# Optimization experiments

Hardware: AMD Instinct MI355X
Metric: run time of the kernel (lower is better)

Reference implementation:

```python
import jax, jax.numpy as jnp
import numpy as np

HEADS = 8
DIM_HEAD = 64
SCALE = DIM_HEAD ** -0.5

B, N, DIM = 4096, 16, 512  # (batch*spatial, frames, channels)
HIDDEN = HEADS * DIM_HEAD  # 512


def setup_inputs() -> dict:
    key = jax.random.key(0)
    k1, k2, k3 = jax.random.split(key, 3)
    x = jax.random.normal(k1, (B, N, DIM), dtype=jnp.float32)
    # torch Linear(dim, 3*hidden, bias=False) applied as x @ W^T; we store the
    # transposed weight directly so forward is x @ w_qkv.
    w_qkv = jax.random.normal(k2, (DIM, 3 * HIDDEN), dtype=jnp.float32) * (DIM ** -0.5)
    w_out = jax.random.normal(k3, (HIDDEN, DIM), dtype=jnp.float32) * (HIDDEN ** -0.5)
    return {"x": x, "w_qkv": w_qkv, "w_out": w_out}


def reference(x, w_qkv, w_out):
    # qkv projection and split
    qkv = x @ w_qkv                                   # [b, n, 3*hidden]
    q, k, v = jnp.split(qkv, 3, axis=-1)              # each [b, n, hidden]

    def to_heads(t):
        b, n, _ = t.shape
        return t.reshape(b, n, HEADS, DIM_HEAD).transpose(0, 2, 1, 3)  # [b, h, n, d]

    q, k, v = to_heads(q), to_heads(k), to_heads(v)

    # linear attention feature maps
    q = jax.nn.softmax(q, axis=-1) * SCALE            # softmax over d
    k = jax.nn.softmax(k, axis=-2)                    # softmax over n

    # context = k^T v : [b, h, d, e]
    context = jnp.einsum('bhnd,bhne->bhde', k, v)
    out = jnp.einsum('bhnd,bhde->bhne', q, context)   # [b, h, n, e]

    b = out.shape[0]
    out = out.transpose(0, 2, 1, 3).reshape(b, N, HIDDEN)  # [b, n, hidden]
    return out @ w_out
```

## Files before the change

### kernel.cpp

```cpp
#include <hip/hip_runtime.h>
#include <hip/hip_bf16.h>


typedef __attribute__((ext_vector_type(8))) short bf16x8;
typedef __attribute__((ext_vector_type(4))) float f32x4;

__device__ __forceinline__ unsigned short f2bf(float f) {
  __hip_bfloat16 h = __float2bfloat16(f);
  return __builtin_bit_cast(unsigned short, h);
}
__device__ __forceinline__ float bf2f(unsigned short u) {
  unsigned int v = ((unsigned int)u) << 16;
  return __builtin_bit_cast(float, v);
}
__device__ __forceinline__ void gload16(const void* g, void* l) {
  __builtin_amdgcn_global_load_lds(
      (__attribute__((address_space(1))) void*)g,
      (__attribute__((address_space(3))) void*)l, 16, 0, 0);
}

__global__ __launch_bounds__(256) void conv_x_k(const float* __restrict__ x,
                                                unsigned short* __restrict__ xb) {
  size_t i = ((size_t)blockIdx.x * 256 + threadIdx.x) * 8;
  float4 a = *(const float4*)(x + i);
  float4 b = *(const float4*)(x + i + 4);
  union { unsigned short u[8]; bf16x8 v; } o;
  o.u[0] = f2bf(a.x); o.u[1] = f2bf(a.y); o.u[2] = f2bf(a.z); o.u[3] = f2bf(a.w);
  o.u[4] = f2bf(b.x); o.u[5] = f2bf(b.y); o.u[6] = f2bf(b.z); o.u[7] = f2bf(b.w);
  *(bf16x8*)(xb + i) = o.v;
}

__global__ __launch_bounds__(256) void conv_w_k(const float* __restrict__ wq,
                                                const float* __restrict__ wo,
                                                unsigned short* __restrict__ wqt,
                                                unsigned short* __restrict__ wot) {
  int i = blockIdx.x * 256 + threadIdx.x;
  if (i < 786432) {
    int n = i >> 9, k = i & 511;
    wqt[i] = f2bf(wq[k * 1536 + n]);
  } else {
    int j = i - 786432;
    int n = j >> 9, k = j & 511;
    wot[j] = f2bf(wo[k * 512 + n]);
  }
}

__global__ __launch_bounds__(256) void gemm_qkv_k(const unsigned short* __restrict__ A,
                                                  const unsigned short* __restrict__ B,
                                                  unsigned short* __restrict__ C) {
  __shared__ __align__(16) unsigned short As[128 * 32];
  __shared__ __align__(16) unsigned short Bs[128 * 32];
  int orig = blockIdx.x;
  int local = orig >> 3;
  int mtile = (orig & 7) * 64 + local / 12;
  int ntile = local % 12;
  int m0 = mtile * 128, n0 = ntile * 128;
  int tid = threadIdx.x, w = tid >> 6, l = tid & 63;
  int wr = w >> 1, wc = w & 1;

  f32x4 z4 = {0.f, 0.f, 0.f, 0.f};
  f32x4 acc[4][4];
#pragma unroll
  for (int i = 0; i < 4; ++i)
#pragma unroll
    for (int j = 0; j < 4; ++j) acc[i][j] = z4;

  const unsigned short* ga0 = A + (size_t)(m0 + w * 32 + (l >> 2)) * 512 + (l & 3) * 8;
  const unsigned short* gb0 = B + (size_t)(n0 + w * 32 + (l >> 2)) * 512 + (l & 3) * 8;
  unsigned short* lA = &As[(w * 32) * 32];
  unsigned short* lB = &Bs[(w * 32) * 32];

  for (int kb = 0; kb < 16; ++kb) {
    if (kb) __syncthreads();
    const unsigned short* ga = ga0 + kb * 32;
    const unsigned short* gb = gb0 + kb * 32;
    gload16(ga, lA);
    gload16(ga + 16 * 512, lA + 16 * 32);
    gload16(gb, lB);
    gload16(gb + 16 * 512, lB + 16 * 32);
    __syncthreads();

    bf16x8 af[4], bfr[4];
#pragma unroll
    for (int mt = 0; mt < 4; ++mt)
      af[mt] = *(const bf16x8*)&As[(wr * 64 + mt * 16 + (l & 15)) * 32 + (l >> 4) * 8];
#pragma unroll
    for (int nt = 0; nt < 4; ++nt)
      bfr[nt] = *(const bf16x8*)&Bs[(wc * 64 + nt * 16 + (l & 15)) * 32 + (l >> 4) * 8];
#pragma unroll
    for (int mt = 0; mt < 4; ++mt)
#pragma unroll
      for (int nt = 0; nt < 4; ++nt)
        acc[mt][nt] = __builtin_amdgcn_mfma_f32_16x16x32_bf16(af[mt], bfr[nt], acc[mt][nt], 0, 0, 0);
  }

#pragma unroll
  for (int mt = 0; mt < 4; ++mt)
#pragma unroll
    for (int nt = 0; nt < 4; ++nt)
#pragma unroll
      for (int r = 0; r < 4; ++r) {
        int row = m0 + wr * 64 + mt * 16 + (l >> 4) * 4 + r;
        int col = n0 + wc * 64 + nt * 16 + (l & 15);
        C[(size_t)row * 1536 + col] = f2bf(acc[mt][nt][r]);
      }
}

#define QOFF 0
#define KOFF 1152
#define VOFF 2304
#define SOFF 3328
__global__ __launch_bounds__(256) void attn_k(const unsigned short* __restrict__ qkv,
                                              unsigned short* __restrict__ attn) {
  __shared__ __align__(16) unsigned short lds[4 * 3584];
  int tid = threadIdx.x, wid = tid >> 6, l = tid & 63;
  int p = blockIdx.x * 4 + wid;
  int b = p >> 3, h = p & 7;
  unsigned short* W = &lds[wid * 3584];
  const size_t rowb = (size_t)(b * 16) * 1536;

  float kv[16];
#pragma unroll
  for (int n = 0; n < 16; ++n) kv[n] = bf2f(qkv[rowb + n * 1536 + 512 + h * 64 + l]);
  float km = kv[0];
#pragma unroll
  for (int n = 1; n < 16; ++n) km = fmaxf(km, kv[n]);
  float ks = 0.f;
#pragma unroll
  for (int n = 0; n < 16; ++n) { kv[n] = __expf(kv[n] - km); ks += kv[n]; }
  float kinv = 1.f / ks;
#pragma unroll
  for (int n = 0; n < 16; ++n) W[KOFF + n * 72 + l] = f2bf(kv[n] * kinv);

#pragma unroll
  for (int n = 0; n < 16; ++n) {
    float x = bf2f(qkv[rowb + n * 1536 + h * 64 + l]);
    float mx = x;
    mx = fmaxf(mx, __shfl_xor(mx, 1));  mx = fmaxf(mx, __shfl_xor(mx, 2));
    mx = fmaxf(mx, __shfl_xor(mx, 4));  mx = fmaxf(mx, __shfl_xor(mx, 8));
    mx = fmaxf(mx, __shfl_xor(mx, 16)); mx = fmaxf(mx, __shfl_xor(mx, 32));
    float e = __expf(x - mx);
    float s = e;
    s += __shfl_xor(s, 1);  s += __shfl_xor(s, 2);  s += __shfl_xor(s, 4);
    s += __shfl_xor(s, 8);  s += __shfl_xor(s, 16); s += __shfl_xor(s, 32);
    W[QOFF + n * 72 + l] = f2bf(e / s * 0.125f);
  }

  const unsigned short* vp = qkv + rowb + (size_t)(l >> 2) * 1536 + 1024 + h * 64 + (l & 3) * 16;
  bf16x8 v0 = *(const bf16x8*)vp;
  bf16x8 v1 = *(const bf16x8*)(vp + 8);
#pragma unroll
  for (int c = 0; c < 8; ++c)
    W[VOFF + ((l & 3) * 16 + c) * 16 + (l >> 2)] = (unsigned short)v0[c];
#pragma unroll
  for (int c = 0; c < 8; ++c)
    W[VOFF + ((l & 3) * 16 + 8 + c) * 16 + (l >> 2)] = (unsigned short)v1[c];
  __syncthreads();

  f32x4 sacc = {0.f, 0.f, 0.f, 0.f};
#pragma unroll
  for (int kb = 0; kb < 2; ++kb) {
    bf16x8 a  = *(const bf16x8*)&W[QOFF + (l & 15) * 72 + kb * 32 + (l >> 4) * 8];
    bf16x8 bb = *(const bf16x8*)&W[KOFF + (l & 15) * 72 + kb * 32 + (l >> 4) * 8];
    sacc = __builtin_amdgcn_mfma_f32_16x16x32_bf16(a, bb, sacc, 0, 0, 0);
  }
#pragma unroll
  for (int r = 0; r < 4; ++r)
    W[SOFF + ((l >> 4) * 4 + r) * 16 + (l & 15)] = f2bf(sacc[r]);
  __syncthreads();

  bf16x8 zz = {0, 0, 0, 0, 0, 0, 0, 0};
  bf16x8 sa = zz;
  if (l < 32) sa = *(const bf16x8*)&W[SOFF + (l & 15) * 16 + (l >> 4) * 8];
#pragma unroll
  for (int et = 0; et < 4; ++et) {
    bf16x8 vb = zz;
    if (l < 32) vb = *(const bf16x8*)&W[VOFF + (et * 16 + (l & 15)) * 16 + (l >> 4) * 8];
    f32x4 o = {0.f, 0.f, 0.f, 0.f};
    o = __builtin_amdgcn_mfma_f32_16x16x32_bf16(sa, vb, o, 0, 0, 0);
#pragma unroll
    for (int r = 0; r < 4; ++r)
      attn[(size_t)(b * 16 + (l >> 4) * 4 + r) * 512 + h * 64 + et * 16 + (l & 15)] = f2bf(o[r]);
  }
}

__global__ __launch_bounds__(256) void gemm_out_k(const unsigned short* __restrict__ A,
                                                  const unsigned short* __restrict__ B,
                                                  float* __restrict__ C) {
  __shared__ __align__(16) unsigned short As[128 * 32];
  __shared__ __align__(16) unsigned short Bs[128 * 32];
  int orig = blockIdx.x;
  int local = orig >> 3;
  int mtile = (orig & 7) * 64 + local / 4;
  int ntile = local % 4;
  int m0 = mtile * 128, n0 = ntile * 128;
  int tid = threadIdx.x, w = tid >> 6, l = tid & 63;
  int wr = w >> 1, wc = w & 1;

  f32x4 z4 = {0.f, 0.f, 0.f, 0.f};
  f32x4 acc[4][4];
#pragma unroll
  for (int i = 0; i < 4; ++i)
#pragma unroll
    for (int j = 0; j < 4; ++j) acc[i][j] = z4;

  const unsigned short* ga0 = A + (size_t)(m0 + w * 32 + (l >> 2)) * 512 + (l & 3) * 8;
  const unsigned short* gb0 = B + (size_t)(n0 + w * 32 + (l >> 2)) * 512 + (l & 3) * 8;
  unsigned short* lA = &As[(w * 32) * 32];
  unsigned short* lB = &Bs[(w * 32) * 32];

  for (int kb = 0; kb < 16; ++kb) {
    if (kb) __syncthreads();
    const unsigned short* ga = ga0 + kb * 32;
    const unsigned short* gb = gb0 + kb * 32;
    gload16(ga, lA);
    gload16(ga + 16 * 512, lA + 16 * 32);
    gload16(gb, lB);
    gload16(gb + 16 * 512, lB + 16 * 32);
    __syncthreads();

    bf16x8 af[4], bfr[4];
#pragma unroll
    for (int mt = 0; mt < 4; ++mt)
      af[mt] = *(const bf16x8*)&As[(wr * 64 + mt * 16 + (l & 15)) * 32 + (l >> 4) * 8];
#pragma unroll
    for (int nt = 0; nt < 4; ++nt)
      bfr[nt] = *(const bf16x8*)&Bs[(wc * 64 + nt * 16 + (l & 15)) * 32 + (l >> 4) * 8];
#pragma unroll
    for (int mt = 0; mt < 4; ++mt)
#pragma unroll
      for (int nt = 0; nt < 4; ++nt)
        acc[mt][nt] = __builtin_amdgcn_mfma_f32_16x16x32_bf16(af[mt], bfr[nt], acc[mt][nt], 0, 0, 0);
  }

#pragma unroll
  for (int mt = 0; mt < 4; ++mt)
#pragma unroll
    for (int nt = 0; nt < 4; ++nt)
#pragma unroll
      for (int r = 0; r < 4; ++r) {
        int row = m0 + wr * 64 + mt * 16 + (l >> 4) * 4 + r;
        int col = n0 + wc * 64 + nt * 16 + (l & 15);
        C[(size_t)row * 512 + col] = acc[mt][nt][r];
      }
}

extern "C" void kernel_launch(void* const* d_in, const int* in_sizes, int n_in,
                              void* d_out, int out_size, void* d_ws, size_t ws_size,
                              hipStream_t stream) {
  const float* x  = (const float*)d_in[0];
  const float* wq = (const float*)d_in[1];
  const float* wo = (const float*)d_in[2];
  float* out = (float*)d_out;

  unsigned short* xb   = (unsigned short*)d_ws;
  unsigned short* wqt  = xb  + 33554432;
  unsigned short* wot  = wqt + 786432;
  unsigned short* qkv  = wot + 262144;
  unsigned short* attn = xb;

  conv_x_k  <<<16384, 256, 0, stream>>>(x, xb);
  conv_w_k  <<<4096,  256, 0, stream>>>(wq, wo, wqt, wot);
  gemm_qkv_k<<<6144,  256, 0, stream>>>(xb, wqt, qkv);
  attn_k    <<<8192,  256, 0, stream>>>(qkv, attn);
  gemm_out_k<<<2048,  256, 0, stream>>>(attn, wot, out);
}
```

Baseline: 509.6 us.

## Replace both GEMMs with 256x256 double-buffered, swizzled, 8-wave pipelined kernel

Both the QKV and output projections now use one templated GEMM with 256x256 tiles, 512 threads, K-tiles of 64, and double-buffered LDS. The LDS layout is XOR-swizzled to avoid bank conflicts. Async global-to-LDS loads are interleaved with MFMA phases using explicit barriers, waitcnt and setprio. The goal is more reuse per tile and hiding load latency behind MFMAs, at the cost of a 128KB LDS footprint and lower occupancy.

```diff
diff --git a/kernel.cpp b/kernel.cpp
--- a/kernel.cpp
+++ b/kernel.cpp
@@ -45,64 +45,119 @@
   }
 }
 
-__global__ __launch_bounds__(256) void gemm_qkv_k(const unsigned short* __restrict__ A,
-                                                  const unsigned short* __restrict__ B,
-                                                  unsigned short* __restrict__ C) {
-  __shared__ __align__(16) unsigned short As[128 * 32];
-  __shared__ __align__(16) unsigned short Bs[128 * 32];
+#define ABUF0 0
+#define ABUF1 16384
+#define BBUF0 32768
+#define BBUF1 49152
+
+__device__ __forceinline__ void stage_half(const unsigned short* __restrict__ G,
+                                           int grow0, unsigned short* ldsb,
+                                           int tid, int kofs) {
+  int r = tid >> 3;
+  int c = ((tid & 7) ^ (r & 7)) << 3;
+  gload16(G + (size_t)(grow0 + r) * 512 + kofs + c, ldsb + tid * 8);
+  gload16(G + (size_t)(grow0 + 64 + r) * 512 + kofs + c, ldsb + 4096 + tid * 8);
+}
+
+#define RD_A(base, mh, sw)                                                   \
+  _Pragma("unroll") for (int mf = 0; mf < 4; ++mf)                           \
+      aF[mf] = *(const bf16x8*)&lds[(base) + (rowA + (mh)*64 + mf*16) * 64 + (sw)];
+#define RD_B(base, sw)                                                       \
+  _Pragma("unroll") for (int nf = 0; nf < 4; ++nf)                           \
+      bF[nf] = *(const bf16x8*)&lds[(base) + (rowB + nf*16) * 64 + (sw)];
+#define DO_MFMA(mh)                                                          \
+  __builtin_amdgcn_s_setprio(1);                                             \
+  _Pragma("unroll") for (int mf = 0; mf < 4; ++mf)                           \
+  _Pragma("unroll") for (int nf = 0; nf < 4; ++nf)                           \
+      acc[(mh)*4 + mf][nf] = __builtin_amdgcn_mfma_f32_16x16x32_bf16(        \
+          aF[mf], bF[nf], acc[(mh)*4 + mf][nf], 0, 0, 0);                    \
+  __builtin_amdgcn_s_setprio(0);
+#define PBAR() __builtin_amdgcn_s_barrier()
+#define LGKM0()                                          \
+  do {                                                   \
+    asm volatile("s_waitcnt lgkmcnt(0)" ::: "memory");   \
+    __builtin_amdgcn_sched_barrier(0);                   \
+  } while (0)
+#define VM2() asm volatile("s_waitcnt vmcnt(2)" ::: "memory")
+
+template <int NTN, bool OUTBF>
+__global__ __launch_bounds__(512) void gemm8_k(const unsigned short* __restrict__ A,
+                                               const unsigned short* __restrict__ B,
+                                               void* __restrict__ Cv) {
+  __shared__ __align__(16) unsigned short lds[65536];
   int orig = blockIdx.x;
-  int local = orig >> 3;
-  int mtile = (orig & 7) * 64 + local / 12;
-  int ntile = local % 12;
-  int m0 = mtile * 128, n0 = ntile * 128;
-  int tid = threadIdx.x, w = tid >> 6, l = tid & 63;
-  int wr = w >> 1, wc = w & 1;
-
-  f32x4 z4 = {0.f, 0.f, 0.f, 0.f};
-  f32x4 acc[4][4];
-#pragma unroll
-  for (int i = 0; i < 4; ++i)
-#pragma unroll
-    for (int j = 0; j < 4; ++j) acc[i][j] = z4;
-
-  const unsigned short* ga0 = A + (size_t)(m0 + w * 32 + (l >> 2)) * 512 + (l & 3) * 8;
-  const unsigned short* gb0 = B + (size_t)(n0 + w * 32 + (l >> 2)) * 512 + (l & 3) * 8;
-  unsigned short* lA = &As[(w * 32) * 32];
-  unsigned short* lB = &Bs[(w * 32) * 32];
-
-  for (int kb = 0; kb < 16; ++kb) {
-    if (kb) __syncthreads();
-    const unsigned short* ga = ga0 + kb * 32;
-    const unsigned short* gb = gb0 + kb * 32;
-    gload16(ga, lA);
-    gload16(ga + 16 * 512, lA + 16 * 32);
-    gload16(gb, lB);
-    gload16(gb + 16 * 512, lB + 16 * 32);
-    __syncthreads();
-
-    bf16x8 af[4], bfr[4];
-#pragma unroll
-    for (int mt = 0; mt < 4; ++mt)
-      af[mt] = *(const bf16x8*)&As[(wr * 64 + mt * 16 + (l & 15)) * 32 + (l >> 4) * 8];
-#pragma unroll
-    for (int nt = 0; nt < 4; ++nt)
-      bfr[nt] = *(const bf16x8*)&Bs[(wc * 64 + nt * 16 + (l & 15)) * 32 + (l >> 4) * 8];
-#pragma unroll
-    for (int mt = 0; mt < 4; ++mt)
-#pragma unroll
-      for (int nt = 0; nt < 4; ++nt)
-        acc[mt][nt] = __builtin_amdgcn_mfma_f32_16x16x32_bf16(af[mt], bfr[nt], acc[mt][nt], 0, 0, 0);
-  }
-
-#pragma unroll
-  for (int mt = 0; mt < 4; ++mt)
-#pragma unroll
-    for (int nt = 0; nt < 4; ++nt)
+  int id = (orig & 7) * (gridDim.x >> 3) + (orig >> 3);
+  int mt = id / NTN, nt = id % NTN;
+  int m0 = mt * 256, n0 = nt * 256;
+  int tid = threadIdx.x, wid = tid >> 6, l = tid & 63;
+  int wr = wid >> 2, wc = wid & 3;
+  int rowA = wr * 128 + (l & 15);
+  int rowB = wc * 64 + (l & 15);
+  int r7 = l & 7;
+  int sw0 = ((l >> 4) ^ r7) << 3;
+  int sw1 = (((l >> 4) | 4) ^ r7) << 3;
+
+  f32x4 acc[8][4];
+#pragma unroll
+  for (int i = 0; i < 8; ++i)
+#pragma unroll
+    for (int j = 0; j < 4; ++j) acc[i][j] = (f32x4){0.f, 0.f, 0.f, 0.f};
+  bf16x8 aF[4], bF[4];
+
+  stage_half(B, n0,       lds + BBUF0,        tid, 0);
+  stage_half(B, n0 + 128, lds + BBUF0 + 8192, tid, 0);
+  stage_half(A, m0,       lds + ABUF0,        tid, 0);
+  stage_half(A, m0 + 128, lds + ABUF0 + 8192, tid, 0);
+  stage_half(B, n0,       lds + BBUF1,        tid, 64);
+  VM2();
+  PBAR();
+
+  for (int it = 0; it < 4; ++it) {
+    int k1 = (2 * it + 1) * 64;
+    int t2 = 2 * it + 2; if (t2 > 7) t2 = 7;
+    int t3 = 2 * it + 3; if (t3 > 7) t3 = 7;
+    int k2 = t2 * 64, k3 = t3 * 64;
+
+    RD_A(ABUF0, 0, sw0); RD_B(BBUF0, sw0);
+    stage_half(B, n0 + 128, lds + BBUF1 + 8192, tid, k1);
+    PBAR(); LGKM0(); DO_MFMA(0); PBAR();
+    RD_A(ABUF0, 1, sw0);
+    stage_half(A, m0, lds + ABUF1, tid, k1);
+    PBAR(); LGKM0(); DO_MFMA(1); PBAR();
+    RD_A(ABUF0, 0, sw1); RD_B(BBUF0, sw1);
+    stage_half(A, m0 + 128, lds + ABUF1 + 8192, tid, k1);
+    PBAR(); LGKM0(); DO_MFMA(0); PBAR();
+    RD_A(ABUF0, 1, sw1);
+    stage_half(B, n0, lds + BBUF0, tid, k2);
+    VM2();
+    PBAR(); LGKM0(); DO_MFMA(1); PBAR();
+    RD_A(ABUF1, 0, sw0); RD_B(BBUF1, sw0);
+    stage_half(B, n0 + 128, lds + BBUF0 + 8192, tid, k2);
+    PBAR(); LGKM0(); DO_MFMA(0); PBAR();
+    RD_A(ABUF1, 1, sw0);
+    stage_half(A, m0, lds + ABUF0, tid, k2);
+    PBAR(); LGKM0(); DO_MFMA(1); PBAR();
+    RD_A(ABUF1, 0, sw1); RD_B(BBUF1, sw1);
+    stage_half(A, m0 + 128, lds + ABUF0 + 8192, tid, k2);
+    PBAR(); LGKM0(); DO_MFMA(0); PBAR();
+    RD_A(ABUF1, 1, sw1);
+    stage_half(B, n0, lds + BBUF1, tid, k3);
+    VM2();
+    PBAR(); LGKM0(); DO_MFMA(1); PBAR();
+  }
+
+#pragma unroll
+  for (int m = 0; m < 8; ++m)
+#pragma unroll
+    for (int nf = 0; nf < 4; ++nf)
 #pragma unroll
       for (int r = 0; r < 4; ++r) {
-        int row = m0 + wr * 64 + mt * 16 + (l >> 4) * 4 + r;
-        int col = n0 + wc * 64 + nt * 16 + (l & 15);
-        C[(size_t)row * 1536 + col] = f2bf(acc[mt][nt][r]);
+        int row = m0 + wr * 128 + m * 16 + (l >> 4) * 4 + r;
+        int col = n0 + wc * 64 + nf * 16 + (l & 15);
+        if (OUTBF)
+          ((unsigned short*)Cv)[(size_t)row * (NTN * 256) + col] = f2bf(acc[m][nf][r]);
+        else
+          ((float*)Cv)[(size_t)row * (NTN * 256) + col] = acc[m][nf][r];
       }
 }
 
@@ -184,67 +239,6 @@
   }
 }
 
-__global__ __launch_bounds__(256) void gemm_out_k(const unsigned short* __restrict__ A,
-                                                  const unsigned short* __restrict__ B,
-                                                  float* __restrict__ C) {
-  __shared__ __align__(16) unsigned short As[128 * 32];
-  __shared__ __align__(16) unsigned short Bs[128 * 32];
-  int orig = blockIdx.x;
-  int local = orig >> 3;
-  int mtile = (orig & 7) * 64 + local / 4;
-  int ntile = local % 4;
-  int m0 = mtile * 128, n0 = ntile * 128;
-  int tid = threadIdx.x, w = tid >> 6, l = tid & 63;
-  int wr = w >> 1, wc = w & 1;
-
-  f32x4 z4 = {0.f, 0.f, 0.f, 0.f};
-  f32x4 acc[4][4];
-#pragma unroll
-  for (int i = 0; i < 4; ++i)
-#pragma unroll
-    for (int j = 0; j < 4; ++j) acc[i][j] = z4;
-
-  const unsigned short* ga0 = A + (size_t)(m0 + w * 32 + (l >> 2)) * 512 + (l & 3) * 8;
-  const unsigned short* gb0 = B + (size_t)(n0 + w * 32 + (l >> 2)) * 512 + (l & 3) * 8;
-  unsigned short* lA = &As[(w * 32) * 32];
-  unsigned short* lB = &Bs[(w * 32) * 32];
-
-  for (int kb = 0; kb < 16; ++kb) {
-    if (kb) __syncthreads();
-    const unsigned short* ga = ga0 + kb * 32;
-    const unsigned short* gb = gb0 + kb * 32;
-    gload16(ga, lA);
-    gload16(ga + 16 * 512, lA + 16 * 32);
-    gload16(gb, lB);
-    gload16(gb + 16 * 512, lB + 16 * 32);
-    __syncthreads();
-
-    bf16x8 af[4], bfr[4];
-#pragma unroll
-    for (int mt = 0; mt < 4; ++mt)
-      af[mt] = *(const bf16x8*)&As[(wr * 64 + mt * 16 + (l & 15)) * 32 + (l >> 4) * 8];
-#pragma unroll
-    for (int nt = 0; nt < 4; ++nt)
-      bfr[nt] = *(const bf16x8*)&Bs[(wc * 64 + nt * 16 + (l & 15)) * 32 + (l >> 4) * 8];
-#pragma unroll
-    for (int mt = 0; mt < 4; ++mt)
-#pragma unroll
-      for (int nt = 0; nt < 4; ++nt)
-        acc[mt][nt] = __builtin_amdgcn_mfma_f32_16x16x32_bf16(af[mt], bfr[nt], acc[mt][nt], 0, 0, 0);
-  }
-
-#pragma unroll
-  for (int mt = 0; mt < 4; ++mt)
-#pragma unroll
-    for (int nt = 0; nt < 4; ++nt)
-#pragma unroll
-      for (int r = 0; r < 4; ++r) {
-        int row = m0 + wr * 64 + mt * 16 + (l >> 4) * 4 + r;
-        int col = n0 + wc * 64 + nt * 16 + (l & 15);
-        C[(size_t)row * 512 + col] = acc[mt][nt][r];
-      }
-}
-
 extern "C" void kernel_launch(void* const* d_in, const int* in_sizes, int n_in,
                               void* d_out, int out_size, void* d_ws, size_t ws_size,
                               hipStream_t stream) {
@@ -259,9 +253,9 @@
   unsigned short* qkv  = wot + 262144;
   unsigned short* attn = xb;
 
-  conv_x_k  <<<16384, 256, 0, stream>>>(x, xb);
-  conv_w_k  <<<4096,  256, 0, stream>>>(wq, wo, wqt, wot);
-  gemm_qkv_k<<<6144,  256, 0, stream>>>(xb, wqt, qkv);
-  attn_k    <<<8192,  256, 0, stream>>>(qkv, attn);
-  gemm_out_k<<<2048,  256, 0, stream>>>(attn, wot, out);
-}
+  conv_x_k<<<16384, 256, 0, stream>>>(x, xb);
+  conv_w_k<<<4096,  256, 0, stream>>>(wq, wo, wqt, wot);
+  gemm8_k<6, true><<<1536, 512, 0, stream>>>(xb, wqt, qkv);
+  attn_k<<<8192, 256, 0, stream>>>(qkv, attn);
+  gemm8_k<2, false><<<512, 512, 0, stream>>>(attn, wot, out);
+}
```

New measurement: 512.3 us. No clear change (+0.5%).
